# Kernel optimization log

Hardware: AMD Instinct MI355X
Metric: run time of the kernel (lower is better)

The kernel has to match this reference:

```python
import jax, jax.numpy as jnp
import numpy as np

N_SAMPLES, N_HORIZON, N_DOF, N_LINKS = 2048, 128, 7, 9
BASE_MASS, EEF_MASS = 100000.0, 243.66


def _constants():
    mass = jnp.array([105.98, 105.98, 314.98, 279.2, 105.98, 105.98, 243.66], jnp.float32)
    total_mass = jnp.sum(mass) + BASE_MASS + EEF_MASS
    diags = np.array([
        [12.19, 12.19, 3.061],
        [12.19, 12.19, 3.061],
        [15.41, 2094.71, 2103.19],
        [9.522, 1966.28, 1966.28],
        [8.305, 3.061, 8.0386],
        [12.13, 12.13, 3.061],
        [9.336, 44.41, 44.41],
    ], np.float32)
    inertial = jnp.asarray(np.stack([np.diag(d) for d in diags]))  # (7,3,3)
    I0 = jnp.diag(jnp.array([69585.02, 69585.02, 66666.664], jnp.float32))
    # base_com_pose = (tf_link0 @ com_link0_local)[:3,3] * eef_mass/(base+eef)
    base_com = jnp.array([0.0, 0.0, 6.65], jnp.float32) * (243.66 / (100000.0 + 243.66))
    return mass, total_mass, inertial, I0, base_com


def _skew(p):
    # p: (...,3) -> (...,3,3)
    x, y, z = p[..., 0], p[..., 1], p[..., 2]
    o = jnp.zeros_like(x)
    return jnp.stack([
        jnp.stack([o, -z, y], -1),
        jnp.stack([z, o, -x], -1),
        jnp.stack([-y, x, o], -1),
    ], -2)


def _inv3(M):
    # analytic 3x3 inverse (batched)
    a, b, c = M[..., 0, 0], M[..., 0, 1], M[..., 0, 2]
    d, e, f = M[..., 1, 0], M[..., 1, 1], M[..., 1, 2]
    g, h, i = M[..., 2, 0], M[..., 2, 1], M[..., 2, 2]
    A = e * i - f * h
    B = f * g - d * i
    C = d * h - e * g
    det = a * A + b * B + c * C
    inv = jnp.stack([
        jnp.stack([A, c * h - b * i, b * f - c * e], -1),
        jnp.stack([B, a * i - c * g, c * d - a * f], -1),
        jnp.stack([C, b * g - a * h, a * e - b * d], -1),
    ], -2)
    return inv / det[..., None, None]


def setup_inputs() -> dict:
    key = jax.random.key(0)
    k1, k2, k3 = jax.random.split(key, 3)
    com_list = jax.random.normal(k1, (N_SAMPLES, N_HORIZON, 3, N_DOF), jnp.float32)
    link_pose_list = jax.random.normal(k2, (N_SAMPLES, N_HORIZON, 4, 4, N_LINKS), jnp.float32)
    jacobian = jax.random.normal(k3, (N_SAMPLES, N_HORIZON, 6, N_DOF), jnp.float32)
    return {"com_list": com_list, "link_pose_list": link_pose_list, "jacobian": jacobian}


def reference(com_list, link_pose_list, jacobian):
    mass, total_mass, inertial, I0, base_com = _constants()
    tril = jnp.tril(jnp.ones((N_DOF, N_DOF), jnp.float32))
    mass_tril = tril * mass[:, None]  # [i,j] = mass_i if j<=i else 0

    # system COM (mass-weighted manipulator COM over total system mass)
    system_com = jnp.einsum('bhci,i->bhc', com_list, mass) / total_mass  # (b,h,3)
    r_og = system_com - base_com                                          # (b,h,3)
    S_og = _skew(r_og)                                                    # (b,h,3,3)

    Jt = jnp.swapaxes(jacobian[:, :, :3, :], -1, -2)                      # (b,h,j=7,3)
    rp = com_list - link_pose_list[:, :, :3, 3, :N_DOF]                   # (b,h,3,i=7)
    rpt = jnp.swapaxes(rp, -1, -2)                                        # (b,h,i=7,3)

    # cross(J_r[j], r_p[i]) for all (i,j): (b,h,7,7,3)
    cross_all = jnp.cross(Jt[:, :, None, :, :], rpt[:, :, :, None, :])

    # J_tw[c,j] = sum_i mass_tril[i,j] * cross_all[i,j,c]
    J_tw = jnp.einsum('bhijc,ij->bhcj', cross_all, mass_tril)             # (b,h,3,7)

    # (p.p) I - p p^T
    r2 = jnp.sum(r_og * r_og, -1)
    skew_mul = r2[..., None, None] * jnp.eye(3, dtype=r_og.dtype) - r_og[..., :, None] * r_og[..., None, :]
    H_w = jnp.sum(inertial, 0) + jnp.sum(mass) * skew_mul + I0            # (b,h,3,3)

    r_oi = com_list - base_com[:, None]                                   # (b,h,3,7)
    S_oi = _skew(jnp.swapaxes(r_oi, -1, -2))                              # (b,h,7,3,3)

    Hwp1 = jnp.einsum('iad,ij,bhjd->bhaj', inertial, tril, Jt)
    Hwp2 = jnp.einsum('bhiac,bhijc,ij->bhaj', S_oi, cross_all, mass_tril)
    H_theta = Hwp1 + Hwp2 - jnp.einsum('bhij,bhjk->bhik', S_og, J_tw)     # (b,h,3,7)

    H_s = total_mass * jnp.matmul(S_og, S_og) + H_w
    H_s_inv = _inv3(H_s)

    top = -(J_tw / total_mass + jnp.matmul(jnp.matmul(S_og, H_s_inv), H_theta))
    bot = -jnp.matmul(H_s_inv, H_theta)
    return jnp.concatenate([top, bot], axis=-2)                            # (b,h,6,7)
```

## Files before the change

kernel.cpp:

```cpp
#include <hip/hip_runtime.h>

#define TPB 64
#define NITEMS (2048*128)

__global__ __launch_bounds__(TPB) void canadarm_kernel(
    const float* __restrict__ com_g,
    const float* __restrict__ pose_g,
    const float* __restrict__ jac_g,
    float* __restrict__ out_g)
{
    __shared__ float sh[TPB*42];
    const int tid = threadIdx.x;
    const size_t item0 = (size_t)blockIdx.x * TPB;
    const size_t item  = item0 + tid;

    const float* C  = com_g  + item*21;
    const float* P  = pose_g + item*144;
    const float* Jg = jac_g  + item*42;

    float com[21];
    #pragma unroll
    for (int k = 0; k < 21; ++k) com[k] = C[k];

    const float mass[7] = {105.98f,105.98f,314.98f,279.2f,105.98f,105.98f,243.66f};
    const float diag[7][3] = {
        {12.19f,12.19f,3.061f},
        {12.19f,12.19f,3.061f},
        {15.41f,2094.71f,2103.19f},
        {9.522f,1966.28f,1966.28f},
        {8.305f,3.061f,8.0386f},
        {12.13f,12.13f,3.061f},
        {9.336f,44.41f,44.41f}};
    float msum = 0.f;
    #pragma unroll
    for (int i = 0; i < 7; ++i) msum += mass[i];
    const float M_total = msum + 100000.0f + 243.66f;
    const float inv_M   = 1.0f / M_total;
    const float bcz     = 6.65f * (243.66f / (100000.0f + 243.66f));
    float Cd[3];
    #pragma unroll
    for (int a = 0; a < 3; ++a) {
        float s0 = 0.f;
        #pragma unroll
        for (int i = 0; i < 7; ++i) s0 += diag[i][a];
        Cd[a] = s0;
    }
    Cd[0] += 69585.02f; Cd[1] += 69585.02f; Cd[2] += 66666.664f;
    const float Kc = M_total - msum;

    float rg[3];
    #pragma unroll
    for (int c = 0; c < 3; ++c) {
        float s0 = 0.f;
        #pragma unroll
        for (int i = 0; i < 7; ++i) s0 += com[c*7+i]*mass[i];
        rg[c] = s0 * inv_M;
    }
    rg[2] -= bcz;

    const float r2 = rg[0]*rg[0] + rg[1]*rg[1] + rg[2]*rg[2];
    const float Hs00 = Kc*(rg[0]*rg[0] - r2) + Cd[0];
    const float Hs11 = Kc*(rg[1]*rg[1] - r2) + Cd[1];
    const float Hs22 = Kc*(rg[2]*rg[2] - r2) + Cd[2];
    const float Hs01 = Kc*rg[0]*rg[1];
    const float Hs02 = Kc*rg[0]*rg[2];
    const float Hs12 = Kc*rg[1]*rg[2];
    const float A = Hs11*Hs22 - Hs12*Hs12;
    const float B = Hs12*Hs02 - Hs01*Hs22;
    const float Cc = Hs01*Hs12 - Hs11*Hs02;
    const float det = Hs00*A + Hs01*B + Hs02*Cc;
    const float id_ = 1.0f/det;
    const float Hi00 = A*id_, Hi01 = B*id_, Hi02 = Cc*id_;
    const float Hi11 = (Hs00*Hs22 - Hs02*Hs02)*id_;
    const float Hi12 = (Hs02*Hs01 - Hs00*Hs12)*id_;
    const float Hi22 = (Hs00*Hs11 - Hs01*Hs01)*id_;

    float w0=0.f,w1=0.f,w2=0.f, ssum=0.f;
    float M00=0.f,M01=0.f,M02=0.f,M10=0.f,M11=0.f,M12=0.f,M20=0.f,M21=0.f,M22=0.f;
    float Ds0=0.f, Ds1=0.f, Ds2=0.f;
    float* O = sh + tid*42;
    #pragma unroll
    for (int j = 6; j >= 0; --j) {
        const float px = P[0*36 + 27 + j];
        const float py = P[1*36 + 27 + j];
        const float pz = P[2*36 + 27 + j];
        const float jx = Jg[0*7 + j];
        const float jy = Jg[1*7 + j];
        const float jz = Jg[2*7 + j];

        const float ax = com[0*7+j] - px;
        const float ay = com[1*7+j] - py;
        const float az = com[2*7+j] - pz;
        const float bxr = com[0*7+j];
        const float byr = com[1*7+j];
        const float bzr = com[2*7+j] - bcz;

        const float mi = mass[j];
        w0 += mi*ax; w1 += mi*ay; w2 += mi*az;
        ssum += mi*(ax*bxr + ay*byr + az*bzr);
        M00 += mi*ax*bxr; M01 += mi*ax*byr; M02 += mi*ax*bzr;
        M10 += mi*ay*bxr; M11 += mi*ay*byr; M12 += mi*ay*bzr;
        M20 += mi*az*bxr; M21 += mi*az*byr; M22 += mi*az*bzr;
        Ds0 += diag[j][0]; Ds1 += diag[j][1]; Ds2 += diag[j][2];

        const float tx = jy*w2 - jz*w1;
        const float ty = jz*w0 - jx*w2;
        const float tz = jx*w1 - jy*w0;

        const float h2x = jx*ssum - (M00*jx + M01*jy + M02*jz);
        const float h2y = jy*ssum - (M10*jx + M11*jy + M12*jz);
        const float h2z = jz*ssum - (M20*jx + M21*jy + M22*jz);

        const float cx = rg[1]*tz - rg[2]*ty;
        const float cy = rg[2]*tx - rg[0]*tz;
        const float cz = rg[0]*ty - rg[1]*tx;

        const float hx = Ds0*jx + h2x - cx;
        const float hy = Ds1*jy + h2y - cy;
        const float hz = Ds2*jz + h2z - cz;

        const float vx = Hi00*hx + Hi01*hy + Hi02*hz;
        const float vy = Hi01*hx + Hi11*hy + Hi12*hz;
        const float vz = Hi02*hx + Hi12*hy + Hi22*hz;
        const float bx = -vx, by = -vy, bz = -vz;

        O[0*7+j] = -tx*inv_M + (rg[1]*bz - rg[2]*by);
        O[1*7+j] = -ty*inv_M + (rg[2]*bx - rg[0]*bz);
        O[2*7+j] = -tz*inv_M + (rg[0]*by - rg[1]*bx);
        O[3*7+j] = bx;
        O[4*7+j] = by;
        O[5*7+j] = bz;
    }
    __syncthreads();

    {
        const float2* so = (const float2*)sh;
        float2* dst = (float2*)(out_g + item0*42);
        #pragma unroll
        for (int i = 0; i < 21; ++i) {
            int p = tid + i*64;
            dst[p] = so[p];
        }
    }
}

extern "C" void kernel_launch(void* const* d_in, const int* in_sizes, int n_in,
                              void* d_out, int out_size, void* d_ws, size_t ws_size,
                              hipStream_t stream) {
    const float* com  = (const float*)d_in[0];
    const float* pose = (const float*)d_in[1];
    const float* jac  = (const float*)d_in[2];
    float* out = (float*)d_out;
    dim3 grid(NITEMS/TPB), block(TPB);
    hipLaunchKernelGGL(canadarm_kernel, grid, block, 0, stream, com, pose, jac, out);
}
```

Measured before the change: 266.7 us.

## Stage inputs into LDS via coalesced global_load_lds before per-thread compute

Replaces strided per-thread global reads of com, jacobian and the pose translation rows with cooperative 16-byte global_load_lds transfers that fill shared memory in coalesced chunks. For the pose tensor, only the last-row region of the first three rows of each item is fetched instead of touching all 144 floats. Threads then read their operands from LDS, and the output staging reuses the jacobian region. This adds a barrier and a larger LDS footprint per block, which may reduce occupancy.

Result: no change. 263.7 us (-1.1%).

```diff
diff --git a/kernel.cpp b/kernel.cpp
--- a/kernel.cpp
+++ b/kernel.cpp
@@ -2,6 +2,16 @@
 
 #define TPB 64
 #define NITEMS (2048*128)
+
+#define COM0  0
+#define JAC0  1344
+#define POSE0 4032
+#define LDS_FLOATS 6336
+
+__device__ __forceinline__ void gload16(void* lds_dst, const void* gsrc) {
+    __builtin_amdgcn_global_load_lds((const __attribute__((address_space(1))) void*)gsrc,
+                                     (__attribute__((address_space(3))) void*)lds_dst, 16, 0, 0);
+}
 
 __global__ __launch_bounds__(TPB) void canadarm_kernel(
     const float* __restrict__ com_g,
@@ -9,18 +19,62 @@
     const float* __restrict__ jac_g,
     float* __restrict__ out_g)
 {
-    __shared__ float sh[TPB*42];
+    __shared__ float sh[LDS_FLOATS];
     const int tid = threadIdx.x;
     const size_t item0 = (size_t)blockIdx.x * TPB;
-    const size_t item  = item0 + tid;
-
-    const float* C  = com_g  + item*21;
-    const float* P  = pose_g + item*144;
-    const float* Jg = jac_g  + item*42;
+
+    {
+        const float* src = com_g + item0*21;
+        #pragma unroll
+        for (int i = 0; i < 5; ++i)
+            gload16(&sh[COM0 + i*256], src + (size_t)(i*64 + tid)*4);
+        if (tid < 16)
+            gload16(&sh[COM0 + 5*256], src + (size_t)(320 + tid)*4);
+    }
+    {
+        const float* src = jac_g + item0*42;
+        #pragma unroll
+        for (int i = 0; i < 10; ++i)
+            gload16(&sh[JAC0 + i*256], src + (size_t)(i*64 + tid)*4);
+        if (tid < 32)
+            gload16(&sh[JAC0 + 10*256], src + (size_t)(640 + tid)*4);
+    }
+    {
+        const float* src = pose_g + item0*144;
+        #pragma unroll
+        for (int i = 0; i < 9; ++i) {
+            const int q   = i*64 + tid;
+            const int it  = q / 9;
+            const int c   = q - it*9;
+            const int run = c / 3;
+            const int e   = c - run*3;
+            gload16(&sh[POSE0 + i*256], src + (size_t)it*144 + run*36 + e*4 + 24);
+        }
+    }
+    __syncthreads();
 
     float com[21];
-    #pragma unroll
-    for (int k = 0; k < 21; ++k) com[k] = C[k];
+    {
+        const float* Lc = sh + COM0 + tid*21;
+        #pragma unroll
+        for (int k = 0; k < 21; ++k) com[k] = Lc[k];
+    }
+    float J3[3][7];
+    {
+        const float* Lj = sh + JAC0 + tid*42;
+        #pragma unroll
+        for (int c = 0; c < 3; ++c)
+            #pragma unroll
+            for (int i = 0; i < 7; ++i) J3[c][i] = Lj[c*7 + i];
+    }
+    float pp[3][7];
+    {
+        const float* Lp = sh + POSE0 + tid*36;
+        #pragma unroll
+        for (int c = 0; c < 3; ++c)
+            #pragma unroll
+            for (int l = 0; l < 7; ++l) pp[c][l] = Lp[c*12 + 3 + l];
+    }
 
     const float mass[7] = {105.98f,105.98f,314.98f,279.2f,105.98f,105.98f,243.66f};
     const float diag[7][3] = {
@@ -78,19 +132,12 @@
     float w0=0.f,w1=0.f,w2=0.f, ssum=0.f;
     float M00=0.f,M01=0.f,M02=0.f,M10=0.f,M11=0.f,M12=0.f,M20=0.f,M21=0.f,M22=0.f;
     float Ds0=0.f, Ds1=0.f, Ds2=0.f;
-    float* O = sh + tid*42;
+    float* O = sh + JAC0 + tid*42;
     #pragma unroll
     for (int j = 6; j >= 0; --j) {
-        const float px = P[0*36 + 27 + j];
-        const float py = P[1*36 + 27 + j];
-        const float pz = P[2*36 + 27 + j];
-        const float jx = Jg[0*7 + j];
-        const float jy = Jg[1*7 + j];
-        const float jz = Jg[2*7 + j];
-
-        const float ax = com[0*7+j] - px;
-        const float ay = com[1*7+j] - py;
-        const float az = com[2*7+j] - pz;
+        const float ax = com[0*7+j] - pp[0][j];
+        const float ay = com[1*7+j] - pp[1][j];
+        const float az = com[2*7+j] - pp[2][j];
         const float bxr = com[0*7+j];
         const float byr = com[1*7+j];
         const float bzr = com[2*7+j] - bcz;
@@ -103,6 +150,7 @@
         M20 += mi*az*bxr; M21 += mi*az*byr; M22 += mi*az*bzr;
         Ds0 += diag[j][0]; Ds1 += diag[j][1]; Ds2 += diag[j][2];
 
+        const float jx = J3[0][j], jy = J3[1][j], jz = J3[2][j];
         const float tx = jy*w2 - jz*w1;
         const float ty = jz*w0 - jx*w2;
         const float tz = jx*w1 - jy*w0;
@@ -134,11 +182,11 @@
     __syncthreads();
 
     {
-        const float2* so = (const float2*)sh;
+        const float2* so = (const float2*)(sh + JAC0);
         float2* dst = (float2*)(out_g + item0*42);
         #pragma unroll
         for (int i = 0; i < 21; ++i) {
-            int p = tid + i*64;
+            const int p = tid + i*64;
             dst[p] = so[p];
         }
     }
```
